# Optimization experiments

Hardware: AMD Instinct MI355X
Metric: run time of the kernel (lower is better)

Reference implementation:

```python
import jax, jax.numpy as jnp
import numpy as np

BN_EPS = 1e-5
NUM_GRAPHS = 64


def _gin_layer(x, src, dst, eps, w1, b1, gamma, beta, w2, b2):
    # GIN aggregation: sum of source features into destination nodes
    n = x.shape[0]
    agg = jax.ops.segment_sum(x[src], dst, num_segments=n)  # [N, d]
    h = (1.0 + eps) * x + agg
    # MLP: Linear -> BatchNorm1d (batch stats, train mode) -> ReLU -> Linear
    h = h @ w1 + b1
    mu = jnp.mean(h, axis=0)
    var = jnp.var(h, axis=0)
    h = gamma * (h - mu) * jax.lax.rsqrt(var + BN_EPS) + beta
    h = jax.nn.relu(h)
    return h @ w2 + b2


def setup_inputs() -> dict:
    key = jax.random.key(0)
    ks = jax.random.split(key, 16)
    N, E, F = 100000, 3200000, 128
    x = jax.random.normal(ks[0], (N, F), dtype=jnp.float32)
    edge_index = jax.random.randint(ks[1], (2, E), 0, N, dtype=jnp.int64)
    batch = jnp.sort(jax.random.randint(ks[2], (N,), 0, NUM_GRAPHS, dtype=jnp.int64))

    def lin(k, fin, fout):
        kw, kb = jax.random.split(k)
        s = 1.0 / np.sqrt(fin)
        w = jax.random.uniform(kw, (fin, fout), jnp.float32, -s, s)
        b = jax.random.uniform(kb, (fout,), jnp.float32, -s, s)
        return w, b

    w1a, b1a = lin(ks[3], F, 64)
    w1b, b1b = lin(ks[4], 64, 32)
    w2a, b2a = lin(ks[5], 32, 64)
    w2b, b2b = lin(ks[6], 64, 16)
    lw, lb = lin(ks[7], 16, 1)
    return {
        "x": x, "edge_index": edge_index, "batch": batch,
        "eps1": jnp.float32(0.0), "eps2": jnp.float32(0.0),
        "w1a": w1a, "b1a": b1a, "g1": jnp.ones(64, jnp.float32), "bt1": jnp.zeros(64, jnp.float32),
        "w1b": w1b, "b1b": b1b,
        "w2a": w2a, "b2a": b2a, "g2": jnp.ones(64, jnp.float32), "bt2": jnp.zeros(64, jnp.float32),
        "w2b": w2b, "b2b": b2b,
        "lw": lw, "lb": lb,
    }


def reference(x, edge_index, batch, eps1, eps2, w1a, b1a, g1, bt1, w1b, b1b,
              w2a, b2a, g2, bt2, w2b, b2b, lw, lb):
    src, dst = edge_index[0], edge_index[1]
    h = _gin_layer(x, src, dst, eps1, w1a, b1a, g1, bt1, w1b, b1b)   # [N, 32]
    h = _gin_layer(h, src, dst, eps2, w2a, b2a, g2, bt2, w2b, b2b)   # [N, 16]
    # global mean pool over graphs
    sums = jax.ops.segment_sum(h, batch, num_segments=NUM_GRAPHS)    # [G, 16]
    counts = jax.ops.segment_sum(jnp.ones((h.shape[0],), h.dtype), batch,
                                 num_segments=NUM_GRAPHS)
    pooled = sums / jnp.maximum(counts, 1.0)[:, None]
    return jax.nn.sigmoid(pooled @ lw + lb)                           # [G, 1]
```

## Files before the change

kernel.cpp:

```cpp
#include <hip/hip_runtime.h>
#include <hip/hip_fp16.h>
#include <math.h>

#define G_GRAPHS 64
#define BIN_SHIFT 7
#define BIN_SIZE 128
#define NBINS_CAP 1024
#define C_CHUNK 16384

__device__ __forceinline__ void fma4(float4& a, float s, float4 w) {
    a.x += s * w.x; a.y += s * w.y; a.z += s * w.z; a.w += s * w.w;
}
__device__ __forceinline__ float4 h4_to_f4(ushort4 u) {
    return make_float4(__half2float(__ushort_as_half(u.x)),
                       __half2float(__ushort_as_half(u.y)),
                       __half2float(__ushort_as_half(u.z)),
                       __half2float(__ushort_as_half(u.w)));
}
__device__ __forceinline__ ushort4 f4_to_h4(float4 f) {
    ushort4 u;
    u.x = __half_as_ushort(__float2half_rn(f.x));
    u.y = __half_as_ushort(__float2half_rn(f.y));
    u.z = __half_as_ushort(__float2half_rn(f.z));
    u.w = __half_as_ushort(__float2half_rn(f.w));
    return u;
}

__device__ __forceinline__ float4 fp8x4_to_f4(unsigned int w) {
#if __has_builtin(__builtin_amdgcn_cvt_f32_fp8)
    float4 r;
    r.x = __builtin_amdgcn_cvt_f32_fp8((int)w, 0);
    r.y = __builtin_amdgcn_cvt_f32_fp8((int)w, 1);
    r.z = __builtin_amdgcn_cvt_f32_fp8((int)w, 2);
    r.w = __builtin_amdgcn_cvt_f32_fp8((int)w, 3);
    return r;
#else
    const float sc = 1.329227995784916e+36f;
    unsigned b0 = w & 0xffu, b1 = (w >> 8) & 0xffu,
             b2 = (w >> 16) & 0xffu, b3 = (w >> 24) & 0xffu;
    float4 r;
    r.x = __uint_as_float(((b0 & 0x80u) << 24) | ((b0 & 0x7fu) << 20)) * sc;
    r.y = __uint_as_float(((b1 & 0x80u) << 24) | ((b1 & 0x7fu) << 20)) * sc;
    r.z = __uint_as_float(((b2 & 0x80u) << 24) | ((b2 & 0x7fu) << 20)) * sc;
    r.w = __uint_as_float(((b3 & 0x80u) << 24) | ((b3 & 0x7fu) << 20)) * sc;
    return r;
#endif
}
__device__ __forceinline__ unsigned int f4_to_fp8x4(float4 f) {
#if __has_builtin(__builtin_amdgcn_cvt_pk_fp8_f32)
    int v = __builtin_amdgcn_cvt_pk_fp8_f32(f.x, f.y, 0, false);
    v = __builtin_amdgcn_cvt_pk_fp8_f32(f.z, f.w, v, true);
    return (unsigned int)v;
#else
    const float sc = 7.52316384526264e-37f;
    float vv[4] = {f.x, f.y, f.z, f.w};
    unsigned out = 0;
    #pragma unroll
    for (int i = 0; i < 4; ++i) {
        unsigned u = __float_as_uint(vv[i] * sc);
        unsigned s = (u >> 24) & 0x80u;
        u += 0x00080000u;
        unsigned m = (u >> 20) & 0x7fu;
        out |= (s | m) << (8 * i);
    }
    return out;
#endif
}

__global__ __launch_bounds__(256) void k_binA(
    const int* __restrict__ dst, int* __restrict__ hist, int nE, int nbins,
    int vec4ok)
{
    __shared__ int cnt[NBINS_CAP];
    for (int i = threadIdx.x; i < nbins; i += 256) cnt[i] = 0;
    __syncthreads();
    int base = blockIdx.x * C_CHUNK;
    int end  = min(base + C_CHUNK, nE);
    int done = base;
    if (vec4ok) {
        int cnt4 = (end - base) >> 2;
        const int4* d4 = (const int4*)(dst + base);
        for (int i = threadIdx.x; i < cnt4; i += 256) {
            int4 v = d4[i];
            atomicAdd(&cnt[v.x >> BIN_SHIFT], 1);
            atomicAdd(&cnt[v.y >> BIN_SHIFT], 1);
            atomicAdd(&cnt[v.z >> BIN_SHIFT], 1);
            atomicAdd(&cnt[v.w >> BIN_SHIFT], 1);
        }
        done = base + (cnt4 << 2);
    }
    for (int e = done + threadIdx.x; e < end; e += 256)
        atomicAdd(&cnt[dst[e] >> BIN_SHIFT], 1);
    __syncthreads();
    int* hrow = hist + (size_t)blockIdx.x * nbins;
    for (int i = threadIdx.x; i < nbins; i += 256) hrow[i] = cnt[i];
}

__global__ __launch_bounds__(256) void k_binB1(
    int* __restrict__ hist, int cblocks, int nbins, int* __restrict__ binCnt)
{
    __shared__ int sb[256];
    int b = blockIdx.x;
    int t = threadIdx.x;
    int v = (t < cblocks) ? hist[(size_t)t * nbins + b] : 0;
    sb[t] = v;
    __syncthreads();
    for (int d = 1; d < 256; d <<= 1) {
        int tt = (t >= d) ? sb[t - d] : 0;
        __syncthreads();
        sb[t] += tt;
        __syncthreads();
    }
    if (t < cblocks) hist[(size_t)t * nbins + b] = sb[t] - v;
    if (t == 0) binCnt[b] = sb[255];
}

__global__ __launch_bounds__(1024) void k_binB2(
    const int* __restrict__ binCnt, int nbins, int nE,
    int* __restrict__ binOff, int* __restrict__ off, int n)
{
    __shared__ int sb[1024];
    int tid = threadIdx.x;
    int v = (tid < nbins) ? binCnt[tid] : 0;
    sb[tid] = v;
    __syncthreads();
    for (int d = 1; d < 1024; d <<= 1) {
        int t = (tid >= d) ? sb[tid - d] : 0;
        __syncthreads();
        sb[tid] += t;
        __syncthreads();
    }
    if (tid < nbins) binOff[tid] = sb[tid] - v;
    if (tid == 0) { binOff[nbins] = nE; off[n] = nE; }
}

__global__ __launch_bounds__(256) void k_binC2(
    const int* __restrict__ src, const int* __restrict__ dst,
    const int* __restrict__ binOff, const int* __restrict__ hist,
    int* __restrict__ staging, int nE, int nbins, int vec4ok)
{
    __shared__ int cnt[NBINS_CAP];
    const int* hrow = hist + (size_t)blockIdx.x * nbins;
    for (int i = threadIdx.x; i < nbins; i += 256)
        cnt[i] = binOff[i] + hrow[i];
    __syncthreads();
    int base = blockIdx.x * C_CHUNK;
    int end  = min(base + C_CHUNK, nE);
    int done = base;
    if (vec4ok) {
        int cnt4 = (end - base) >> 2;
        const int4* d4 = (const int4*)(dst + base);
        const int4* s4 = (const int4*)(src + base);
        for (int i = threadIdx.x; i < cnt4; i += 256) {
            int4 dv = d4[i]; int4 sv = s4[i];
            int b, p;
            b = dv.x >> BIN_SHIFT; p = atomicAdd(&cnt[b], 1);
            staging[p] = ((dv.x & (BIN_SIZE-1)) << 17) | sv.x;
            b = dv.y >> BIN_SHIFT; p = atomicAdd(&cnt[b], 1);
            staging[p] = ((dv.y & (BIN_SIZE-1)) << 17) | sv.y;
            b = dv.z >> BIN_SHIFT; p = atomicAdd(&cnt[b], 1);
            staging[p] = ((dv.z & (BIN_SIZE-1)) << 17) | sv.z;
            b = dv.w >> BIN_SHIFT; p = atomicAdd(&cnt[b], 1);
            staging[p] = ((dv.w & (BIN_SIZE-1)) << 17) | sv.w;
        }
        done = base + (cnt4 << 2);
    }
    for (int e = done + threadIdx.x; e < end; e += 256) {
        int d = dst[e], s = src[e];
        int b = d >> BIN_SHIFT;
        int p = atomicAdd(&cnt[b], 1);
        staging[p] = ((d & (BIN_SIZE - 1)) << 17) | s;
    }
}

__global__ __launch_bounds__(256) void k_binD(
    const int* __restrict__ binOff, const int* __restrict__ staging,
    int* __restrict__ off, int* __restrict__ csr, int n)
{
    __shared__ int deg[BIN_SIZE];
    __shared__ int cur[BIN_SIZE];
    int b = blockIdx.x;
    int s = binOff[b], e = binOff[b + 1];
    int tid = threadIdx.x;
    if (tid < BIN_SIZE) deg[tid] = 0;
    __syncthreads();
    for (int j = s + tid; j < e; j += 256)
        atomicAdd(&deg[staging[j] >> 17], 1);
    __syncthreads();
    if (tid < BIN_SIZE) cur[tid] = deg[tid];
    __syncthreads();
    for (int d = 1; d < BIN_SIZE; d <<= 1) {
        int t = (tid >= d && tid < BIN_SIZE) ? cur[tid - d] : 0;
        __syncthreads();
        if (tid < BIN_SIZE) cur[tid] += t;
        __syncthreads();
    }
    if (tid < BIN_SIZE) {
        int node = b * BIN_SIZE + tid;
        int ex = s + cur[tid] - deg[tid];
        if (node < n) off[node] = ex;
        cur[tid] = ex;
    }
    __syncthreads();
    for (int j = s + tid; j < e; j += 256) {
        int pk = staging[j];
        int p = atomicAdd(&cur[pk >> 17], 1);
        csr[p] = pk & 0x1FFFF;
    }
}

__global__ __launch_bounds__(256) void k_gemm1(
    const float* __restrict__ x, const float* __restrict__ w1a,
    unsigned int* __restrict__ y8, int n)
{
    __shared__ float  xs[64 * 129];
    __shared__ float4 ws[128 * 16];
    int tid = threadIdx.x;
    const float4* w4 = (const float4*)w1a;
    #pragma unroll
    for (int i = tid; i < 128 * 16; i += 256) ws[i] = w4[i];
    int row0 = blockIdx.x * 64;
    for (int i = tid; i < 64 * 32; i += 256) {
        int r = i >> 5, k4 = i & 31;
        float4 v = {0.f, 0.f, 0.f, 0.f};
        if (row0 + r < n) v = ((const float4*)x)[(size_t)(row0 + r) * 32 + k4];
        xs[r * 129 + k4 * 4 + 0] = v.x;
        xs[r * 129 + k4 * 4 + 1] = v.y;
        xs[r * 129 + k4 * 4 + 2] = v.z;
        xs[r * 129 + k4 * 4 + 3] = v.w;
    }
    __syncthreads();
    int c4 = tid & 15, rg = tid >> 4;
    float4 acc[4] = {{0,0,0,0},{0,0,0,0},{0,0,0,0},{0,0,0,0}};
    const float* xr = xs + rg * 4 * 129;
    #pragma unroll 8
    for (int k = 0; k < 128; ++k) {
        float4 wv = ws[k * 16 + c4];
        fma4(acc[0], xr[k +   0], wv);
        fma4(acc[1], xr[k + 129], wv);
        fma4(acc[2], xr[k + 258], wv);
        fma4(acc[3], xr[k + 387], wv);
    }
    #pragma unroll
    for (int i = 0; i < 4; ++i) {
        int row = row0 + rg * 4 + i;
        if (row < n) y8[(size_t)row * 16 + c4] = f4_to_fp8x4(acc[i]);
    }
}

__global__ __launch_bounds__(256) void k_agg1(
    const unsigned int* __restrict__ y8, const int* __restrict__ off,
    const int* __restrict__ csr, const float* __restrict__ b1a,
    const float* __restrict__ eps1p, __half* __restrict__ h1, int n,
    float* __restrict__ p_sum, float* __restrict__ p_sq)
{
    __shared__ float s_sum[4][64];
    __shared__ float s_sq[4][64];
    int slot = threadIdx.x >> 6;
    int lane = threadIdx.x & 63;
    int node = blockIdx.x * 4 + slot;
    int c = lane & 15;
    int g = lane >> 4;
    bool valid = node < n;
    int o = 0, e = 0;
    if (valid) { o = off[node]; e = off[node + 1]; }
    float4 acc = {0.f, 0.f, 0.f, 0.f};
    float4 acc2 = {0.f, 0.f, 0.f, 0.f};
    if (valid && g == 0) {
        float4 v = fp8x4_to_f4(y8[(size_t)node * 16 + c]);
        float4 bv = ((const float4*)b1a)[c];
        float ep = 1.0f + eps1p[0];
        acc.x = ep * v.x + bv.x; acc.y = ep * v.y + bv.y;
        acc.z = ep * v.z + bv.z; acc.w = ep * v.w + bv.w;
    }
    int j = o + g;
    for (; j + 12 < e; j += 16) {
        int s0 = csr[j], s1 = csr[j + 4], s2 = csr[j + 8], s3 = csr[j + 12];
        unsigned w0 = y8[(size_t)s0 * 16 + c];
        unsigned w1 = y8[(size_t)s1 * 16 + c];
        unsigned w2 = y8[(size_t)s2 * 16 + c];
        unsigned w3 = y8[(size_t)s3 * 16 + c];
        float4 v0 = fp8x4_to_f4(w0);
        float4 v1 = fp8x4_to_f4(w1);
        float4 v2 = fp8x4_to_f4(w2);
        float4 v3 = fp8x4_to_f4(w3);
        acc.x  += v0.x + v1.x; acc.y  += v0.y + v1.y;
        acc.z  += v0.z + v1.z; acc.w  += v0.w + v1.w;
        acc2.x += v2.x + v3.x; acc2.y += v2.y + v3.y;
        acc2.z += v2.z + v3.z; acc2.w += v2.w + v3.w;
    }
    for (; j < e; j += 4) {
        float4 v = fp8x4_to_f4(y8[(size_t)csr[j] * 16 + c]);
        acc.x += v.x; acc.y += v.y; acc.z += v.z; acc.w += v.w;
    }
    acc.x += acc2.x; acc.y += acc2.y; acc.z += acc2.z; acc.w += acc2.w;
    acc.x += __shfl_xor(acc.x, 16, 64); acc.x += __shfl_xor(acc.x, 32, 64);
    acc.y += __shfl_xor(acc.y, 16, 64); acc.y += __shfl_xor(acc.y, 32, 64);
    acc.z += __shfl_xor(acc.z, 16, 64); acc.z += __shfl_xor(acc.z, 32, 64);
    acc.w += __shfl_xor(acc.w, 16, 64); acc.w += __shfl_xor(acc.w, 32, 64);
    if (g == 0) {
        if (valid) ((ushort4*)h1)[(size_t)node * 16 + c] = f4_to_h4(acc);
        float vx = valid ? acc.x : 0.f, vy = valid ? acc.y : 0.f;
        float vz = valid ? acc.z : 0.f, vw = valid ? acc.w : 0.f;
        s_sum[slot][4*c+0] = vx; s_sum[slot][4*c+1] = vy;
        s_sum[slot][4*c+2] = vz; s_sum[slot][4*c+3] = vw;
        s_sq[slot][4*c+0] = vx*vx; s_sq[slot][4*c+1] = vy*vy;
        s_sq[slot][4*c+2] = vz*vz; s_sq[slot][4*c+3] = vw*vw;
    }
    __syncthreads();
    if (threadIdx.x < 64) {
        int col = threadIdx.x;
        float s = s_sum[0][col] + s_sum[1][col] + s_sum[2][col] + s_sum[3][col];
        float q = s_sq[0][col]  + s_sq[1][col]  + s_sq[2][col]  + s_sq[3][col];
        int ps = (blockIdx.x & 63) * 64 + col;
        atomicAdd(&p_sum[ps], s);
        atomicAdd(&p_sq[ps], q);
    }
}

__global__ __launch_bounds__(256) void k_agg2(
    const unsigned int* __restrict__ h28, const int* __restrict__ off,
    const int* __restrict__ csr, const float* __restrict__ eps2p,
    __half* __restrict__ agg2h, int n)
{
    int node = blockIdx.x * 4 + (threadIdx.x >> 6);
    if (node >= n) return;
    int lane = threadIdx.x & 63;
    int c = lane & 7;
    int g = lane >> 3;
    int o = off[node], e = off[node + 1];
    float4 acc = {0.f, 0.f, 0.f, 0.f};
    float4 acc2 = {0.f, 0.f, 0.f, 0.f};
    if (g == 0) {
        float4 v = fp8x4_to_f4(h28[(size_t)node * 8 + c]);
        float ep = 1.0f + eps2p[0];
        acc.x = ep * v.x; acc.y = ep * v.y; acc.z = ep * v.z; acc.w = ep * v.w;
    }
    int j = o + g;
    for (; j + 24 < e; j += 32) {
        int s0 = csr[j], s1 = csr[j + 8], s2 = csr[j + 16], s3 = csr[j + 24];
        unsigned w0 = h28[(size_t)s0 * 8 + c];
        unsigned w1 = h28[(size_t)s1 * 8 + c];
        unsigned w2 = h28[(size_t)s2 * 8 + c];
        unsigned w3 = h28[(size_t)s3 * 8 + c];
        float4 v0 = fp8x4_to_f4(w0);
        float4 v1 = fp8x4_to_f4(w1);
        float4 v2 = fp8x4_to_f4(w2);
        float4 v3 = fp8x4_to_f4(w3);
        acc.x  += v0.x + v1.x; acc.y  += v0.y + v1.y;
        acc.z  += v0.z + v1.z; acc.w  += v0.w + v1.w;
        acc2.x += v2.x + v3.x; acc2.y += v2.y + v3.y;
        acc2.z += v2.z + v3.z; acc2.w += v2.w + v3.w;
    }
    for (; j < e; j += 8) {
        float4 v = fp8x4_to_f4(h28[(size_t)csr[j] * 8 + c]);
        acc.x += v.x; acc.y += v.y; acc.z += v.z; acc.w += v.w;
    }
    acc.x += acc2.x; acc.y += acc2.y; acc.z += acc2.z; acc.w += acc2.w;
    acc.x += __shfl_xor(acc.x, 8, 64); acc.x += __shfl_xor(acc.x, 16, 64); acc.x += __shfl_xor(acc.x, 32, 64);
    acc.y += __shfl_xor(acc.y, 8, 64); acc.y += __shfl_xor(acc.y, 16, 64); acc.y += __shfl_xor(acc.y, 32, 64);
    acc.z += __shfl_xor(acc.z, 8, 64); acc.z += __shfl_xor(acc.z, 16, 64); acc.z += __shfl_xor(acc.z, 32, 64);
    acc.w += __shfl_xor(acc.w, 8, 64); acc.w += __shfl_xor(acc.w, 16, 64); acc.w += __shfl_xor(acc.w, 32, 64);
    if (g == 0)
        ((ushort4*)agg2h)[(size_t)node * 8 + c] = f4_to_h4(acc);
}

__global__ void k_bnfin(const float* __restrict__ p_sum, const float* __restrict__ p_sq,
                        const float* __restrict__ gamma, const float* __restrict__ beta,
                        float nf, float* __restrict__ a, float* __restrict__ c)
{
    int i = threadIdx.x;
    float s = 0.f, q = 0.f;
    for (int k = 0; k < 64; ++k) { s += p_sum[k*64 + i]; q += p_sq[k*64 + i]; }
    float mu  = s / nf;
    float var = q / nf - mu * mu;
    float av  = gamma[i] * rsqrtf(var + 1e-5f);
    a[i] = av;
    c[i] = beta[i] - av * mu;
}

__global__ __launch_bounds__(256) void k_mlp1b(
    const __half* __restrict__ h1, const float* __restrict__ a1,
    const float* __restrict__ c1, const float* __restrict__ w1b,
    const float* __restrict__ b1b, unsigned int* __restrict__ h28, int n)
{
    __shared__ float  xs[128 * 65];
    __shared__ float4 ws[64 * 8];
    __shared__ float  as[64], cs[64];
    int tid = threadIdx.x;
    #pragma unroll
    for (int i = tid; i < 64 * 8; i += 256) ws[i] = ((const float4*)w1b)[i];
    if (tid < 64) { as[tid] = a1[tid]; cs[tid] = c1[tid]; }
    __syncthreads();
    int row0 = blockIdx.x * 128;
    for (int i = tid; i < 128 * 16; i += 256) {
        int r = i >> 4, k4 = i & 15;
        float4 v = {0.f, 0.f, 0.f, 0.f};
        if (row0 + r < n) {
            v = h4_to_f4(((const ushort4*)h1)[(size_t)(row0 + r) * 16 + k4]);
            v.x = fmaxf(as[k4*4+0] * v.x + cs[k4*4+0], 0.f);
            v.y = fmaxf(as[k4*4+1] * v.y + cs[k4*4+1], 0.f);
            v.z = fmaxf(as[k4*4+2] * v.z + cs[k4*4+2], 0.f);
            v.w = fmaxf(as[k4*4+3] * v.w + cs[k4*4+3], 0.f);
        }
        xs[r * 65 + k4 * 4 + 0] = v.x;
        xs[r * 65 + k4 * 4 + 1] = v.y;
        xs[r * 65 + k4 * 4 + 2] = v.z;
        xs[r * 65 + k4 * 4 + 3] = v.w;
    }
    __syncthreads();
    int c4 = tid & 7, rg = tid >> 3;
    float4 bv = ((const float4*)b1b)[c4];
    float4 acc[4] = {bv, bv, bv, bv};
    const float* xr = xs + rg * 4 * 65;
    #pragma unroll 8
    for (int k = 0; k < 64; ++k) {
        float4 wv = ws[k * 8 + c4];
        fma4(acc[0], xr[k +   0], wv);
        fma4(acc[1], xr[k +  65], wv);
        fma4(acc[2], xr[k + 130], wv);
        fma4(acc[3], xr[k + 195], wv);
    }
    #pragma unroll
    for (int i = 0; i < 4; ++i) {
        int row = row0 + rg * 4 + i;
        if (row < n) h28[(size_t)row * 8 + c4] = f4_to_fp8x4(acc[i]);
    }
}

__global__ __launch_bounds__(256) void k_gemm2(
    const __half* __restrict__ agg2h, const float* __restrict__ w2a,
    const float* __restrict__ b2a, __half* __restrict__ h3, int n,
    float* __restrict__ p_sum, float* __restrict__ p_sq)
{
    __shared__ float  xs[64 * 33];
    __shared__ float4 ws[32 * 16];
    __shared__ float  s_sum[64], s_sq[64];
    int tid = threadIdx.x;
    if (tid < 64) { s_sum[tid] = 0.f; s_sq[tid] = 0.f; }
    #pragma unroll
    for (int i = tid; i < 32 * 16; i += 256) ws[i] = ((const float4*)w2a)[i];
    int row0 = blockIdx.x * 64;
    for (int i = tid; i < 64 * 8; i += 256) {
        int r = i >> 3, k4 = i & 7;
        float4 v = {0.f, 0.f, 0.f, 0.f};
        if (row0 + r < n) v = h4_to_f4(((const ushort4*)agg2h)[(size_t)(row0 + r) * 8 + k4]);
        xs[r * 33 + k4 * 4 + 0] = v.x;
        xs[r * 33 + k4 * 4 + 1] = v.y;
        xs[r * 33 + k4 * 4 + 2] = v.z;
        xs[r * 33 + k4 * 4 + 3] = v.w;
    }
    __syncthreads();
    int c4 = tid & 15, rg = tid >> 4;
    float4 bv = ((const float4*)b2a)[c4];
    float4 acc[4] = {bv, bv, bv, bv};
    const float* xr = xs + rg * 4 * 33;
    #pragma unroll
    for (int k = 0; k < 32; ++k) {
        float4 wv = ws[k * 16 + c4];
        fma4(acc[0], xr[k +  0], wv);
        fma4(acc[1], xr[k + 33], wv);
        fma4(acc[2], xr[k + 66], wv);
        fma4(acc[3], xr[k + 99], wv);
    }
    float cs_[4] = {0,0,0,0}, cq_[4] = {0,0,0,0};
    #pragma unroll
    for (int i = 0; i < 4; ++i) {
        int row = row0 + rg * 4 + i;
        if (row < n) {
            ((ushort4*)h3)[(size_t)row * 16 + c4] = f4_to_h4(acc[i]);
            cs_[0] += acc[i].x; cq_[0] += acc[i].x * acc[i].x;
            cs_[1] += acc[i].y; cq_[1] += acc[i].y * acc[i].y;
            cs_[2] += acc[i].z; cq_[2] += acc[i].z * acc[i].z;
            cs_[3] += acc[i].w; cq_[3] += acc[i].w * acc[i].w;
        }
    }
    #pragma unroll
    for (int jj = 0; jj < 4; ++jj) {
        atomicAdd(&s_sum[c4 * 4 + jj], cs_[jj]);
        atomicAdd(&s_sq[c4 * 4 + jj],  cq_[jj]);
    }
    __syncthreads();
    if (tid < 64) {
        int ps = (blockIdx.x & 63) * 64 + tid;
        atomicAdd(&p_sum[ps], s_sum[tid]);
        atomicAdd(&p_sq[ps],  s_sq[tid]);
    }
}

__global__ __launch_bounds__(256) void k_final(
    const __half* __restrict__ h3, const float* __restrict__ a2,
    const float* __restrict__ c2, const float* __restrict__ w2b,
    const float* __restrict__ b2b, const int* __restrict__ batch,
    float* __restrict__ pool, float* __restrict__ cnt, int n)
{
    __shared__ float  xs[64 * 65];
    __shared__ float4 ws[64 * 4];
    __shared__ float  as[64], cs[64];
    __shared__ float  pl[G_GRAPHS * 16];
    __shared__ float  cl[G_GRAPHS];
    int tid = threadIdx.x;
    for (int i = tid; i < 256; i += 256) ws[i] = ((const float4*)w2b)[i];
    if (tid < 64) { as[tid] = a2[tid]; cs[tid] = c2[tid]; cl[tid] = 0.f; }
    for (int i = tid; i < G_GRAPHS * 16; i += 256) pl[i] = 0.f;
    __syncthreads();
    int row0 = blockIdx.x * 64;
    for (int i = tid; i < 64 * 16; i += 256) {
        int r = i >> 4, k4 = i & 15;
        float4 v = {0.f, 0.f, 0.f, 0.f};
        if (row0 + r < n) {
            v = h4_to_f4(((const ushort4*)h3)[(size_t)(row0 + r) * 16 + k4]);
            v.x = fmaxf(as[k4*4+0] * v.x + cs[k4*4+0], 0.f);
            v.y = fmaxf(as[k4*4+1] * v.y + cs[k4*4+1], 0.f);
            v.z = fmaxf(as[k4*4+2] * v.z + cs[k4*4+2], 0.f);
            v.w = fmaxf(as[k4*4+3] * v.w + cs[k4*4+3], 0.f);
        }
        xs[r * 65 + k4 * 4 + 0] = v.x;
        xs[r * 65 + k4 * 4 + 1] = v.y;
        xs[r * 65 + k4 * 4 + 2] = v.z;
        xs[r * 65 + k4 * 4 + 3] = v.w;
    }
    __syncthreads();
    int c4 = tid & 3, r = tid >> 2;
    float4 acc = ((const float4*)b2b)[c4];
    const float* xr = xs + r * 65;
    #pragma unroll 8
    for (int k = 0; k < 64; ++k) {
        float4 wv = ws[k * 4 + c4];
        fma4(acc, xr[k], wv);
    }
    int row = row0 + r;
    if (row < n) {
        int g = batch[row];
        if (c4 == 0) atomicAdd(&cl[g], 1.f);
        float* pp = &pl[g * 16 + c4 * 4];
        atomicAdd(pp + 0, acc.x); atomicAdd(pp + 1, acc.y);
        atomicAdd(pp + 2, acc.z); atomicAdd(pp + 3, acc.w);
    }
    __syncthreads();
    if (tid < 64 && cl[tid] != 0.f) atomicAdd(&cnt[tid], cl[tid]);
    for (int i = tid; i < G_GRAPHS * 16; i += 256) {
        int g = i >> 4;
        if (cl[g] != 0.f) atomicAdd(&pool[i], pl[i]);
    }
}

__global__ void k_head(const float* __restrict__ pool, const float* __restrict__ cnt,
                       const float* __restrict__ lw, const float* __restrict__ lb,
                       float* __restrict__ out)
{
    int g = threadIdx.x;
    float cv = fmaxf(cnt[g], 1.0f);
    float acc = lb[0];
    #pragma unroll
    for (int f = 0; f < 16; ++f) acc += (pool[g * 16 + f] / cv) * lw[f];
    out[g] = 1.0f / (1.0f + expf(-acc));
}

extern "C" void kernel_launch(void* const* d_in, const int* in_sizes, int n_in,
                              void* d_out, int out_size, void* d_ws, size_t ws_size,
                              hipStream_t stream)
{
    const float* x    = (const float*)d_in[0];
    const int*   eidx = (const int*)d_in[1];
    const int*   batch= (const int*)d_in[2];
    const float* eps1 = (const float*)d_in[3];
    const float* eps2 = (const float*)d_in[4];
    const float* w1a  = (const float*)d_in[5];
    const float* b1a  = (const float*)d_in[6];
    const float* g1   = (const float*)d_in[7];
    const float* bt1  = (const float*)d_in[8];
    const float* w1b  = (const float*)d_in[9];
    const float* b1b  = (const float*)d_in[10];
    const float* w2a  = (const float*)d_in[11];
    const float* b2a  = (const float*)d_in[12];
    const float* g2   = (const float*)d_in[13];
    const float* bt2  = (const float*)d_in[14];
    const float* w2b  = (const float*)d_in[15];
    const float* b2b  = (const float*)d_in[16];
    const float* lw   = (const float*)d_in[17];
    const float* lb   = (const float*)d_in[18];
    float* out = (float*)d_out;

    int n  = in_sizes[0] / 128;
    int nE = in_sizes[1] / 2;
    const int* srcI = eidx;
    const int* dstI = eidx + nE;
    int vec4ok = ((nE & 3) == 0) && ((((uintptr_t)eidx) & 15) == 0);

    char* wsb = (char*)d_ws;
    size_t nn = (size_t)n;
    unsigned int* y8  = (unsigned int*)wsb;
    __half* h1        = (__half*)(wsb + nn * 64);
    unsigned int* h28 = (unsigned int*)(wsb + nn * 192);
    __half* agg2h     = (__half*)(wsb + nn * 224);
    __half* h3        = h1;
    float* stats = (float*)(wsb + nn * 288);
    float* a1     = stats;          float* c1     = stats + 64;
    float* a2     = stats + 128;    float* c2     = stats + 192;
    float* pool   = stats + 256;    float* cntb   = stats + 1280;
    float* p_sum1 = stats + 1344;   float* p_sq1  = stats + 5440;
    float* p_sum2 = stats + 9536;   float* p_sq2  = stats + 13632;

    int cblocks = (nE + C_CHUNK - 1) / C_CHUNK;
    int nbins   = (n + BIN_SIZE - 1) >> BIN_SHIFT;

    int* off     = (int*)(stats + 17728);
    int* csr     = off + (n + 1);
    int* binCnt  = csr + nE;
    int* binOff  = binCnt + NBINS_CAP + 1;
    int* staging = binOff + NBINS_CAP + 1;
    int* hist    = staging + nE;

    hipMemsetAsync(stats + 256, 0, (17728 - 256) * sizeof(float), stream);

    int tiles64  = (n + 63) / 64;
    int tiles128 = (n + 127) / 128;
    int nblocks4 = (n + 3) / 4;

    k_gemm1<<<tiles64, 256, 0, stream>>>(x, w1a, y8, n);

    k_binA<<<cblocks, 256, 0, stream>>>(dstI, hist, nE, nbins, vec4ok);
    k_binB1<<<nbins, 256, 0, stream>>>(hist, cblocks, nbins, binCnt);
    k_binB2<<<1, 1024, 0, stream>>>(binCnt, nbins, nE, binOff, off, n);
    k_binC2<<<cblocks, 256, 0, stream>>>(srcI, dstI, binOff, hist, staging, nE, nbins, vec4ok);
    k_binD<<<nbins, 256, 0, stream>>>(binOff, staging, off, csr, n);

    k_agg1<<<nblocks4, 256, 0, stream>>>(y8, off, csr, b1a, eps1, h1, n, p_sum1, p_sq1);
    k_bnfin<<<1, 64, 0, stream>>>(p_sum1, p_sq1, g1, bt1, (float)n, a1, c1);
    k_mlp1b<<<tiles128, 256, 0, stream>>>(h1, a1, c1, w1b, b1b, h28, n);
    k_agg2<<<nblocks4, 256, 0, stream>>>(h28, off, csr, eps2, agg2h, n);
    k_gemm2<<<tiles64, 256, 0, stream>>>(agg2h, w2a, b2a, h3, n, p_sum2, p_sq2);
    k_bnfin<<<1, 64, 0, stream>>>(p_sum2, p_sq2, g2, bt2, (float)n, a2, c2);
    k_final<<<tiles64, 256, 0, stream>>>(h3, a2, c2, w2b, b2b, batch, pool, cntb, n);
    k_head<<<1, 64, 0, stream>>>(pool, cntb, lw, lb, out);
}
```

Baseline: 297.6 us.

## Merge gemm1 with bin histogram launch and widen per-lane gather loads

The first-layer GEMM and the edge-destination histogram are combined into one launch, with block index ranges picking which job a block does, so the two independent stages can run concurrently and one launch is saved. Separately, both aggregation kernels now have each lane load 8 bytes (8 fp8 values) per neighbour instead of 4, halving the lanes per row so more edges are in flight per wavefront. The results are stored as 16-byte half vectors. Costs: the fused kernel's shared memory is the sum of both parts, which may lower occupancy, and there is one more shuffle reduction step.

```diff
diff --git a/kernel.cpp b/kernel.cpp
--- a/kernel.cpp
+++ b/kernel.cpp
@@ -8,8 +8,13 @@
 #define NBINS_CAP 1024
 #define C_CHUNK 16384
 
+typedef unsigned short usv8 __attribute__((ext_vector_type(8)));
+
 __device__ __forceinline__ void fma4(float4& a, float s, float4 w) {
     a.x += s * w.x; a.y += s * w.y; a.z += s * w.z; a.w += s * w.w;
+}
+__device__ __forceinline__ void add4(float4& a, float4 b) {
+    a.x += b.x; a.y += b.y; a.z += b.z; a.w += b.w;
 }
 __device__ __forceinline__ float4 h4_to_f4(ushort4 u) {
     return make_float4(__half2float(__ushort_as_half(u.x)),
@@ -24,6 +29,18 @@
     u.z = __half_as_ushort(__float2half_rn(f.z));
     u.w = __half_as_ushort(__float2half_rn(f.w));
     return u;
+}
+__device__ __forceinline__ usv8 f4x2_to_h8(float4 a, float4 b) {
+    usv8 r;
+    r.s0 = __half_as_ushort(__float2half_rn(a.x));
+    r.s1 = __half_as_ushort(__float2half_rn(a.y));
+    r.s2 = __half_as_ushort(__float2half_rn(a.z));
+    r.s3 = __half_as_ushort(__float2half_rn(a.w));
+    r.s4 = __half_as_ushort(__float2half_rn(b.x));
+    r.s5 = __half_as_ushort(__float2half_rn(b.y));
+    r.s6 = __half_as_ushort(__float2half_rn(b.z));
+    r.s7 = __half_as_ushort(__float2half_rn(b.w));
+    return r;
 }
 
 __device__ __forceinline__ float4 fp8x4_to_f4(unsigned int w) {
@@ -67,33 +84,72 @@
 #endif
 }
 
-__global__ __launch_bounds__(256) void k_binA(
+__global__ __launch_bounds__(256) void k_g1A(
+    const float* __restrict__ x, const float* __restrict__ w1a,
+    unsigned int* __restrict__ y8, int n, int tiles64,
     const int* __restrict__ dst, int* __restrict__ hist, int nE, int nbins,
     int vec4ok)
 {
-    __shared__ int cnt[NBINS_CAP];
-    for (int i = threadIdx.x; i < nbins; i += 256) cnt[i] = 0;
-    __syncthreads();
-    int base = blockIdx.x * C_CHUNK;
-    int end  = min(base + C_CHUNK, nE);
-    int done = base;
-    if (vec4ok) {
-        int cnt4 = (end - base) >> 2;
-        const int4* d4 = (const int4*)(dst + base);
-        for (int i = threadIdx.x; i < cnt4; i += 256) {
-            int4 v = d4[i];
-            atomicAdd(&cnt[v.x >> BIN_SHIFT], 1);
-            atomicAdd(&cnt[v.y >> BIN_SHIFT], 1);
-            atomicAdd(&cnt[v.z >> BIN_SHIFT], 1);
-            atomicAdd(&cnt[v.w >> BIN_SHIFT], 1);
-        }
-        done = base + (cnt4 << 2);
-    }
-    for (int e = done + threadIdx.x; e < end; e += 256)
-        atomicAdd(&cnt[dst[e] >> BIN_SHIFT], 1);
-    __syncthreads();
-    int* hrow = hist + (size_t)blockIdx.x * nbins;
-    for (int i = threadIdx.x; i < nbins; i += 256) hrow[i] = cnt[i];
+    __shared__ float  xs[64 * 129];
+    __shared__ float4 ws[128 * 16];
+    __shared__ int    cnt[NBINS_CAP];
+    int tid = threadIdx.x;
+    if (blockIdx.x < tiles64) {
+        const float4* w4 = (const float4*)w1a;
+        #pragma unroll
+        for (int i = tid; i < 128 * 16; i += 256) ws[i] = w4[i];
+        int row0 = blockIdx.x * 64;
+        for (int i = tid; i < 64 * 32; i += 256) {
+            int r = i >> 5, k4 = i & 31;
+            float4 v = {0.f, 0.f, 0.f, 0.f};
+            if (row0 + r < n) v = ((const float4*)x)[(size_t)(row0 + r) * 32 + k4];
+            xs[r * 129 + k4 * 4 + 0] = v.x;
+            xs[r * 129 + k4 * 4 + 1] = v.y;
+            xs[r * 129 + k4 * 4 + 2] = v.z;
+            xs[r * 129 + k4 * 4 + 3] = v.w;
+        }
+        __syncthreads();
+        int c4 = tid & 15, rg = tid >> 4;
+        float4 acc[4] = {{0,0,0,0},{0,0,0,0},{0,0,0,0},{0,0,0,0}};
+        const float* xr = xs + rg * 4 * 129;
+        #pragma unroll 8
+        for (int k = 0; k < 128; ++k) {
+            float4 wv = ws[k * 16 + c4];
+            fma4(acc[0], xr[k +   0], wv);
+            fma4(acc[1], xr[k + 129], wv);
+            fma4(acc[2], xr[k + 258], wv);
+            fma4(acc[3], xr[k + 387], wv);
+        }
+        #pragma unroll
+        for (int i = 0; i < 4; ++i) {
+            int row = row0 + rg * 4 + i;
+            if (row < n) y8[(size_t)row * 16 + c4] = f4_to_fp8x4(acc[i]);
+        }
+    } else {
+        int blk = blockIdx.x - tiles64;
+        for (int i = tid; i < nbins; i += 256) cnt[i] = 0;
+        __syncthreads();
+        int base = blk * C_CHUNK;
+        int end  = min(base + C_CHUNK, nE);
+        int done = base;
+        if (vec4ok) {
+            int cnt4 = (end - base) >> 2;
+            const int4* d4 = (const int4*)(dst + base);
+            for (int i = tid; i < cnt4; i += 256) {
+                int4 v = d4[i];
+                atomicAdd(&cnt[v.x >> BIN_SHIFT], 1);
+                atomicAdd(&cnt[v.y >> BIN_SHIFT], 1);
+                atomicAdd(&cnt[v.z >> BIN_SHIFT], 1);
+                atomicAdd(&cnt[v.w >> BIN_SHIFT], 1);
+            }
+            done = base + (cnt4 << 2);
+        }
+        for (int e = done + tid; e < end; e += 256)
+            atomicAdd(&cnt[dst[e] >> BIN_SHIFT], 1);
+        __syncthreads();
+        int* hrow = hist + (size_t)blk * nbins;
+        for (int i = tid; i < nbins; i += 256) hrow[i] = cnt[i];
+    }
 }
 
 __global__ __launch_bounds__(256) void k_binB1(
@@ -209,45 +265,6 @@
     }
 }
 
-__global__ __launch_bounds__(256) void k_gemm1(
-    const float* __restrict__ x, const float* __restrict__ w1a,
-    unsigned int* __restrict__ y8, int n)
-{
-    __shared__ float  xs[64 * 129];
-    __shared__ float4 ws[128 * 16];
-    int tid = threadIdx.x;
-    const float4* w4 = (const float4*)w1a;
-    #pragma unroll
-    for (int i = tid; i < 128 * 16; i += 256) ws[i] = w4[i];
-    int row0 = blockIdx.x * 64;
-    for (int i = tid; i < 64 * 32; i += 256) {
-        int r = i >> 5, k4 = i & 31;
-        float4 v = {0.f, 0.f, 0.f, 0.f};
-        if (row0 + r < n) v = ((const float4*)x)[(size_t)(row0 + r) * 32 + k4];
-        xs[r * 129 + k4 * 4 + 0] = v.x;
-        xs[r * 129 + k4 * 4 + 1] = v.y;
-        xs[r * 129 + k4 * 4 + 2] = v.z;
-        xs[r * 129 + k4 * 4 + 3] = v.w;
-    }
-    __syncthreads();
-    int c4 = tid & 15, rg = tid >> 4;
-    float4 acc[4] = {{0,0,0,0},{0,0,0,0},{0,0,0,0},{0,0,0,0}};
-    const float* xr = xs + rg * 4 * 129;
-    #pragma unroll 8
-    for (int k = 0; k < 128; ++k) {
-        float4 wv = ws[k * 16 + c4];
-        fma4(acc[0], xr[k +   0], wv);
-        fma4(acc[1], xr[k + 129], wv);
-        fma4(acc[2], xr[k + 258], wv);
-        fma4(acc[3], xr[k + 387], wv);
-    }
-    #pragma unroll
-    for (int i = 0; i < 4; ++i) {
-        int row = row0 + rg * 4 + i;
-        if (row < n) y8[(size_t)row * 16 + c4] = f4_to_fp8x4(acc[i]);
-    }
-}
-
 __global__ __launch_bounds__(256) void k_agg1(
     const unsigned int* __restrict__ y8, const int* __restrict__ off,
     const int* __restrict__ csr, const float* __restrict__ b1a,
@@ -259,53 +276,57 @@
     int slot = threadIdx.x >> 6;
     int lane = threadIdx.x & 63;
     int node = blockIdx.x * 4 + slot;
-    int c = lane & 15;
-    int g = lane >> 4;
+    int c = lane & 7;
+    int g = lane >> 3;
     bool valid = node < n;
     int o = 0, e = 0;
     if (valid) { o = off[node]; e = off[node + 1]; }
-    float4 acc = {0.f, 0.f, 0.f, 0.f};
-    float4 acc2 = {0.f, 0.f, 0.f, 0.f};
+    const uint2* y82 = (const uint2*)y8;
+    float4 aLo = {0,0,0,0}, aHi = {0,0,0,0};
     if (valid && g == 0) {
-        float4 v = fp8x4_to_f4(y8[(size_t)node * 16 + c]);
-        float4 bv = ((const float4*)b1a)[c];
+        uint2 v = y82[(size_t)node * 8 + c];
+        float4 lo = fp8x4_to_f4(v.x), hi = fp8x4_to_f4(v.y);
+        float4 b0 = ((const float4*)b1a)[c * 2];
+        float4 b1 = ((const float4*)b1a)[c * 2 + 1];
         float ep = 1.0f + eps1p[0];
-        acc.x = ep * v.x + bv.x; acc.y = ep * v.y + bv.y;
-        acc.z = ep * v.z + bv.z; acc.w = ep * v.w + bv.w;
+        aLo.x = ep * lo.x + b0.x; aLo.y = ep * lo.y + b0.y;
+        aLo.z = ep * lo.z + b0.z; aLo.w = ep * lo.w + b0.w;
+        aHi.x = ep * hi.x + b1.x; aHi.y = ep * hi.y + b1.y;
+        aHi.z = ep * hi.z + b1.z; aHi.w = ep * hi.w + b1.w;
     }
     int j = o + g;
-    for (; j + 12 < e; j += 16) {
-        int s0 = csr[j], s1 = csr[j + 4], s2 = csr[j + 8], s3 = csr[j + 12];
-        unsigned w0 = y8[(size_t)s0 * 16 + c];
-        unsigned w1 = y8[(size_t)s1 * 16 + c];
-        unsigned w2 = y8[(size_t)s2 * 16 + c];
-        unsigned w3 = y8[(size_t)s3 * 16 + c];
-        float4 v0 = fp8x4_to_f4(w0);
-        float4 v1 = fp8x4_to_f4(w1);
-        float4 v2 = fp8x4_to_f4(w2);
-        float4 v3 = fp8x4_to_f4(w3);
-        acc.x  += v0.x + v1.x; acc.y  += v0.y + v1.y;
-        acc.z  += v0.z + v1.z; acc.w  += v0.w + v1.w;
-        acc2.x += v2.x + v3.x; acc2.y += v2.y + v3.y;
-        acc2.z += v2.z + v3.z; acc2.w += v2.w + v3.w;
-    }
-    for (; j < e; j += 4) {
-        float4 v = fp8x4_to_f4(y8[(size_t)csr[j] * 16 + c]);
-        acc.x += v.x; acc.y += v.y; acc.z += v.z; acc.w += v.w;
-    }
-    acc.x += acc2.x; acc.y += acc2.y; acc.z += acc2.z; acc.w += acc2.w;
-    acc.x += __shfl_xor(acc.x, 16, 64); acc.x += __shfl_xor(acc.x, 32, 64);
-    acc.y += __shfl_xor(acc.y, 16, 64); acc.y += __shfl_xor(acc.y, 32, 64);
-    acc.z += __shfl_xor(acc.z, 16, 64); acc.z += __shfl_xor(acc.z, 32, 64);
-    acc.w += __shfl_xor(acc.w, 16, 64); acc.w += __shfl_xor(acc.w, 32, 64);
+    for (; j + 8 < e; j += 16) {
+        int s0 = csr[j], s1 = csr[j + 8];
+        uint2 w0 = y82[(size_t)s0 * 8 + c];
+        uint2 w1 = y82[(size_t)s1 * 8 + c];
+        add4(aLo, fp8x4_to_f4(w0.x)); add4(aHi, fp8x4_to_f4(w0.y));
+        add4(aLo, fp8x4_to_f4(w1.x)); add4(aHi, fp8x4_to_f4(w1.y));
+    }
+    for (; j < e; j += 8) {
+        uint2 w = y82[(size_t)csr[j] * 8 + c];
+        add4(aLo, fp8x4_to_f4(w.x)); add4(aHi, fp8x4_to_f4(w.y));
+    }
+    #pragma unroll
+    for (int d = 8; d < 64; d <<= 1) {
+        aLo.x += __shfl_xor(aLo.x, d, 64); aLo.y += __shfl_xor(aLo.y, d, 64);
+        aLo.z += __shfl_xor(aLo.z, d, 64); aLo.w += __shfl_xor(aLo.w, d, 64);
+        aHi.x += __shfl_xor(aHi.x, d, 64); aHi.y += __shfl_xor(aHi.y, d, 64);
+        aHi.z += __shfl_xor(aHi.z, d, 64); aHi.w += __shfl_xor(aHi.w, d, 64);
+    }
     if (g == 0) {
-        if (valid) ((ushort4*)h1)[(size_t)node * 16 + c] = f4_to_h4(acc);
-        float vx = valid ? acc.x : 0.f, vy = valid ? acc.y : 0.f;
-        float vz = valid ? acc.z : 0.f, vw = valid ? acc.w : 0.f;
-        s_sum[slot][4*c+0] = vx; s_sum[slot][4*c+1] = vy;
-        s_sum[slot][4*c+2] = vz; s_sum[slot][4*c+3] = vw;
-        s_sq[slot][4*c+0] = vx*vx; s_sq[slot][4*c+1] = vy*vy;
-        s_sq[slot][4*c+2] = vz*vz; s_sq[slot][4*c+3] = vw*vw;
+        if (valid) ((usv8*)h1)[(size_t)node * 8 + c] = f4x2_to_h8(aLo, aHi);
+        float v0 = valid ? aLo.x : 0.f, v1 = valid ? aLo.y : 0.f;
+        float v2 = valid ? aLo.z : 0.f, v3 = valid ? aLo.w : 0.f;
+        float v4 = valid ? aHi.x : 0.f, v5 = valid ? aHi.y : 0.f;
+        float v6 = valid ? aHi.z : 0.f, v7 = valid ? aHi.w : 0.f;
+        s_sum[slot][8*c+0] = v0; s_sum[slot][8*c+1] = v1;
+        s_sum[slot][8*c+2] = v2; s_sum[slot][8*c+3] = v3;
+        s_sum[slot][8*c+4] = v4; s_sum[slot][8*c+5] = v5;
+        s_sum[slot][8*c+6] = v6; s_sum[slot][8*c+7] = v7;
+        s_sq[slot][8*c+0] = v0*v0; s_sq[slot][8*c+1] = v1*v1;
+        s_sq[slot][8*c+2] = v2*v2; s_sq[slot][8*c+3] = v3*v3;
+        s_sq[slot][8*c+4] = v4*v4; s_sq[slot][8*c+5] = v5*v5;
+        s_sq[slot][8*c+6] = v6*v6; s_sq[slot][8*c+7] = v7*v7;
     }
     __syncthreads();
     if (threadIdx.x < 64) {
@@ -326,43 +347,39 @@
     int node = blockIdx.x * 4 + (threadIdx.x >> 6);
     if (node >= n) return;
     int lane = threadIdx.x & 63;
-    int c = lane & 7;
-    int g = lane >> 3;
+    int c = lane & 3;
+    int g = lane >> 2;
     int o = off[node], e = off[node + 1];
-    float4 acc = {0.f, 0.f, 0.f, 0.f};
-    float4 acc2 = {0.f, 0.f, 0.f, 0.f};
+    const uint2* h282 = (const uint2*)h28;
+    float4 aLo = {0,0,0,0}, aHi = {0,0,0,0};
     if (g == 0) {
-        float4 v = fp8x4_to_f4(h28[(size_t)node * 8 + c]);
+        uint2 v = h282[(size_t)node * 4 + c];
+        float4 lo = fp8x4_to_f4(v.x), hi = fp8x4_to_f4(v.y);
         float ep = 1.0f + eps2p[0];
-        acc.x = ep * v.x; acc.y = ep * v.y; acc.z = ep * v.z; acc.w = ep * v.w;
+        aLo.x = ep * lo.x; aLo.y = ep * lo.y; aLo.z = ep * lo.z; aLo.w = ep * lo.w;
+        aHi.x = ep * hi.x; aHi.y = ep * hi.y; aHi.z = ep * hi.z; aHi.w = ep * hi.w;
     }
     int j = o + g;
-    for (; j + 24 < e; j += 32) {
-        int s0 = csr[j], s1 = csr[j + 8], s2 = csr[j + 16], s3 = csr[j + 24];
-        unsigned w0 = h28[(size_t)s0 * 8 + c];
-        unsigned w1 = h28[(size_t)s1 * 8 + c];
-        unsigned w2 = h28[(size_t)s2 * 8 + c];
-        unsigned w3 = h28[(size_t)s3 * 8 + c];
-        float4 v0 = fp8x4_to_f4(w0);
-        float4 v1 = fp8x4_to_f4(w1);
-        float4 v2 = fp8x4_to_f4(w2);
-        float4 v3 = fp8x4_to_f4(w3);
-        acc.x  += v0.x + v1.x; acc.y  += v0.y + v1.y;
-        acc.z  += v0.z + v1.z; acc.w  += v0.w + v1.w;
-        acc2.x += v2.x + v3.x; acc2.y += v2.y + v3.y;
-        acc2.z += v2.z + v3.z; acc2.w += v2.w + v3.w;
-    }
-    for (; j < e; j += 8) {
-        float4 v = fp8x4_to_f4(h28[(size_t)csr[j] * 8 + c]);
-        acc.x += v.x; acc.y += v.y; acc.z += v.z; acc.w += v.w;
-    }
-    acc.x += acc2.x; acc.y += acc2.y; acc.z += acc2.z; acc.w += acc2.w;
-    acc.x += __shfl_xor(acc.x, 8, 64); acc.x += __shfl_xor(acc.x, 16, 64); acc.x += __shfl_xor(acc.x, 32, 64);
-    acc.y += __shfl_xor(acc.y, 8, 64); acc.y += __shfl_xor(acc.y, 16, 64); acc.y += __shfl_xor(acc.y, 32, 64);
-    acc.z += __shfl_xor(acc.z, 8, 64); acc.z += __shfl_xor(acc.z, 16, 64); acc.z += __shfl_xor(acc.z, 32, 64);
-    acc.w += __shfl_xor(acc.w, 8, 64); acc.w += __shfl_xor(acc.w, 16, 64); acc.w += __shfl_xor(acc.w, 32, 64);
+    for (; j + 16 < e; j += 32) {
+        int s0 = csr[j], s1 = csr[j + 16];
+        uint2 w0 = h282[(size_t)s0 * 4 + c];
+        uint2 w1 = h282[(size_t)s1 * 4 + c];
+        add4(aLo, fp8x4_to_f4(w0.x)); add4(aHi, fp8x4_to_f4(w0.y));
+        add4(aLo, fp8x4_to_f4(w1.x)); add4(aHi, fp8x4_to_f4(w1.y));
+    }
+    for (; j < e; j += 16) {
+        uint2 w = h282[(size_t)csr[j] * 4 + c];
+        add4(aLo, fp8x4_to_f4(w.x)); add4(aHi, fp8x4_to_f4(w.y));
+    }
+    #pragma unroll
+    for (int d = 4; d < 64; d <<= 1) {
+        aLo.x += __shfl_xor(aLo.x, d, 64); aLo.y += __shfl_xor(aLo.y, d, 64);
+        aLo.z += __shfl_xor(aLo.z, d, 64); aLo.w += __shfl_xor(aLo.w, d, 64);
+        aHi.x += __shfl_xor(aHi.x, d, 64); aHi.y += __shfl_xor(aHi.y, d, 64);
+        aHi.z += __shfl_xor(aHi.z, d, 64); aHi.w += __shfl_xor(aHi.w, d, 64);
+    }
     if (g == 0)
-        ((ushort4*)agg2h)[(size_t)node * 8 + c] = f4_to_h4(acc);
+        ((usv8*)agg2h)[(size_t)node * 4 + c] = f4x2_to_h8(aLo, aHi);
 }
 
 __global__ void k_bnfin(const float* __restrict__ p_sum, const float* __restrict__ p_sq,
@@ -618,9 +635,8 @@
     int tiles128 = (n + 127) / 128;
     int nblocks4 = (n + 3) / 4;
 
-    k_gemm1<<<tiles64, 256, 0, stream>>>(x, w1a, y8, n);
-
-    k_binA<<<cblocks, 256, 0, stream>>>(dstI, hist, nE, nbins, vec4ok);
+    k_g1A<<<tiles64 + cblocks, 256, 0, stream>>>(x, w1a, y8, n, tiles64,
+                                                 dstI, hist, nE, nbins, vec4ok);
     k_binB1<<<nbins, 256, 0, stream>>>(hist, cblocks, nbins, binCnt);
     k_binB2<<<1, 1024, 0, stream>>>(binCnt, nbins, nE, binOff, off, n);
     k_binC2<<<cblocks, 256, 0, stream>>>(srcI, dstI, binOff, hist, staging, nE, nbins, vec4ok);
```

Measured after the change: 278.0 us (median of 2 runs). -6.6%, faster.
